# Kernel tuning notes

Measured on AMD Instinct MI355X. Metric: run time of the kernel, lower is better.

The kernel has to match this reference:

```python
import jax, jax.numpy as jnp
import numpy as np

N_NODES = 50000
N_EDGES = 800000
D = 128


def setup_inputs() -> dict:
    key = jax.random.key(0)
    ks = jax.random.split(key, 6)
    stdv = 1.0 / np.sqrt(D)
    inputs = {
        "input": jax.random.normal(ks[0], (N_NODES, D), dtype=jnp.float32),
        "h0": jax.random.normal(ks[1], (N_NODES, D), dtype=jnp.float32),
        # COO representation of the (normalized) sparse adjacency
        "vals": jax.random.uniform(ks[2], (N_EDGES,), dtype=jnp.float32) / 16.0,
        "weight": jax.random.uniform(ks[3], (D, D), dtype=jnp.float32, minval=-stdv, maxval=stdv),
        "lamda": jnp.float32(0.5),
        "alpha": jnp.float32(0.1),
        "row": jax.random.randint(ks[4], (N_EDGES,), 0, N_NODES),
        "col": jax.random.randint(ks[5], (N_EDGES,), 0, N_NODES),
        "l": 4,
    }
    return inputs


def reference(input, h0, vals, weight, lamda, alpha, row, col, l):
    # theta = log(lamda / l + 1)
    theta = jnp.log(lamda / l + 1.0)
    # hi = spmm(adj, input): gather source-node features, scale by edge
    # values, scatter-add into destination rows.  [E, D] -> [N, D]
    hi = jax.ops.segment_sum(vals[:, None] * input[col], row, num_segments=input.shape[0])
    # variant=False path
    support = (1.0 - alpha) * hi + alpha * h0
    r = support
    # output = theta * support @ W + (1 - theta) * r
    output = theta * jnp.matmul(support, weight) + (1.0 - theta) * r
    return output
```

## Files before the change

### kernel.cpp

```cpp
#include <hip/hip_runtime.h>
#include <cmath>

constexpr int N_NODES = 50000;
constexpr int N_EDGES = 800000;
constexpr int D = 128;
constexpr int CAP = 32;
constexpr int OVF_CAP = 8192;

constexpr int EPB = 2048;
constexpr int SCAT_BLOCKS = (N_EDGES + EPB - 1) / EPB;
constexpr int CAST_BLOCKS = (N_NODES * D / 8 + 255) / 256;

constexpr size_t OFF_OVFCNT = 200000;
constexpr size_t OFF_BUCKET = 200064;
constexpr size_t OFF_OVF    = 6600064;
constexpr size_t OFF_PACKED = 6731136;
constexpr size_t OFF_WT     = 19531136;

typedef __attribute__((ext_vector_type(8))) short bf16x8;
typedef __attribute__((ext_vector_type(4))) float f32x4;

__device__ __forceinline__ unsigned bf16rn(float f) {
    unsigned u = __float_as_uint(f);
    return (u + 0x7fffu + ((u >> 16) & 1u)) >> 16;
}
__device__ __forceinline__ float bf_lo(unsigned u) { return __uint_as_float(u << 16); }
__device__ __forceinline__ float bf_hi(unsigned u) { return __uint_as_float(u & 0xffff0000u); }

__device__ __forceinline__ unsigned enc_val(float v) {
    int m = (int)(v * 1048576.0f + 0.5f);
    if (m > 65535) m = 65535;
    if (m < 0) m = 0;
    return (unsigned)m;
}

__device__ __forceinline__ void push_edge(
    int r, int c, float v,
    int* __restrict__ cnt, unsigned* __restrict__ bucket,
    int* __restrict__ ovf_cnt, int4* __restrict__ ovf)
{
    unsigned ent = (unsigned)c | (enc_val(v) << 16);
    int pos = atomicAdd(&cnt[r], 1);
    if (pos < CAP) bucket[(size_t)r * CAP + pos] = ent;
    else {
        int o = atomicAdd(ovf_cnt, 1);
        if (o < OVF_CAP) ovf[o] = make_int4(r, c,
            __float_as_int((float)(ent >> 16) * (1.0f / 1048576.0f)), 0);
    }
}

__global__ __launch_bounds__(256) void scatter_cast(
    const int* __restrict__ row, const int* __restrict__ col,
    const float* __restrict__ vals, const float* __restrict__ input,
    const float* __restrict__ weight,
    int* __restrict__ cnt, unsigned* __restrict__ bucket,
    int* __restrict__ ovf_cnt, int4* __restrict__ ovf,
    unsigned* __restrict__ packed, ushort* __restrict__ wt)
{
    if (blockIdx.x < SCAT_BLOCKS) {
        const int gbase = blockIdx.x * (EPB / 4);

        #pragma unroll
        for (int it = 0; it < EPB / 4 / 256; ++it) {
            int gi = gbase + it * 256 + threadIdx.x;
            if (gi >= N_EDGES / 4) break;
            int4   r4 = ((const int4*)row)[gi];
            int4   c4 = ((const int4*)col)[gi];
            float4 v4 = ((const float4*)vals)[gi];
            push_edge(r4.x, c4.x, v4.x, cnt, bucket, ovf_cnt, ovf);
            push_edge(r4.y, c4.y, v4.y, cnt, bucket, ovf_cnt, ovf);
            push_edge(r4.z, c4.z, v4.z, cnt, bucket, ovf_cnt, ovf);
            push_edge(r4.w, c4.w, v4.w, cnt, bucket, ovf_cnt, ovf);
        }
    } else if (blockIdx.x < SCAT_BLOCKS + CAST_BLOCKS) {
        int i = (blockIdx.x - SCAT_BLOCKS) * 256 + threadIdx.x;
        if (i >= N_NODES * D / 8) return;
        const float4* f = (const float4*)(input + (size_t)i * 8);
        float4 a = f[0], b = f[1];
        uint4 o;
        o.x = bf16rn(a.x) | (bf16rn(a.y) << 16);
        o.y = bf16rn(a.z) | (bf16rn(a.w) << 16);
        o.z = bf16rn(b.x) | (bf16rn(b.y) << 16);
        o.w = bf16rn(b.z) | (bf16rn(b.w) << 16);
        ((uint4*)packed)[i] = o;
    } else {
        #pragma unroll
        for (int j = 0; j < 64; ++j) {
            int idx = threadIdx.x + j * 256;
            int k = idx >> 7, n = idx & 127;
            wt[n * 128 + k] = (ushort)bf16rn(weight[idx]);
        }
    }
}

__global__ __launch_bounds__(256) void gather_support(
    const unsigned* __restrict__ packed,
    const float* __restrict__ h0,
    const float* __restrict__ alpha_p,
    const int* __restrict__ cnt,
    const unsigned* __restrict__ bucket,
    float* __restrict__ support)
{
    const float alpha = *alpha_p;
    const float oma = 1.0f - alpha;
    const int wv   = threadIdx.x >> 6;
    const int lane = threadIdx.x & 63;
    const int q    = lane & 15;
    const int slot = lane >> 4;

    const int g = blockIdx.x * 4 + wv;
    if (g >= N_NODES) return;

    int n = cnt[g];
    if (n > CAP) n = CAP;
    const unsigned* b = bucket + (size_t)g * CAP;
    const uint4* pk = (const uint4*)packed;

    const int q4 = (n + 3) >> 2;
    const int s0 = slot * q4;
    int s1 = s0 + q4; if (s1 > n) s1 = n;

    float acc[8] = {0.f, 0.f, 0.f, 0.f, 0.f, 0.f, 0.f, 0.f};
    for (int e = s0; e < s1; e += 4) {
        int rem = s1 - e;
        unsigned m0 = b[e];
        unsigned m1 = (rem > 1) ? b[e + 1] : 0u;
        unsigned m2 = (rem > 2) ? b[e + 2] : 0u;
        unsigned m3 = (rem > 3) ? b[e + 3] : 0u;
        uint4 x0 = pk[(size_t)(m0 & 0xffffu) * 16 + q];
        uint4 x1 = pk[(size_t)(m1 & 0xffffu) * 16 + q];
        uint4 x2 = pk[(size_t)(m2 & 0xffffu) * 16 + q];
        uint4 x3 = pk[(size_t)(m3 & 0xffffu) * 16 + q];
        float v0 = (float)(m0 >> 16) * (1.0f / 1048576.0f);
        float v1 = (float)(m1 >> 16) * (1.0f / 1048576.0f);
        float v2 = (float)(m2 >> 16) * (1.0f / 1048576.0f);
        float v3 = (float)(m3 >> 16) * (1.0f / 1048576.0f);
        acc[0] += v0 * bf_lo(x0.x); acc[1] += v0 * bf_hi(x0.x);
        acc[2] += v0 * bf_lo(x0.y); acc[3] += v0 * bf_hi(x0.y);
        acc[4] += v0 * bf_lo(x0.z); acc[5] += v0 * bf_hi(x0.z);
        acc[6] += v0 * bf_lo(x0.w); acc[7] += v0 * bf_hi(x0.w);
        acc[0] += v1 * bf_lo(x1.x); acc[1] += v1 * bf_hi(x1.x);
        acc[2] += v1 * bf_lo(x1.y); acc[3] += v1 * bf_hi(x1.y);
        acc[4] += v1 * bf_lo(x1.z); acc[5] += v1 * bf_hi(x1.z);
        acc[6] += v1 * bf_lo(x1.w); acc[7] += v1 * bf_hi(x1.w);
        acc[0] += v2 * bf_lo(x2.x); acc[1] += v2 * bf_hi(x2.x);
        acc[2] += v2 * bf_lo(x2.y); acc[3] += v2 * bf_hi(x2.y);
        acc[4] += v2 * bf_lo(x2.z); acc[5] += v2 * bf_hi(x2.z);
        acc[6] += v2 * bf_lo(x2.w); acc[7] += v2 * bf_hi(x2.w);
        acc[0] += v3 * bf_lo(x3.x); acc[1] += v3 * bf_hi(x3.x);
        acc[2] += v3 * bf_lo(x3.y); acc[3] += v3 * bf_hi(x3.y);
        acc[4] += v3 * bf_lo(x3.z); acc[5] += v3 * bf_hi(x3.z);
        acc[6] += v3 * bf_lo(x3.w); acc[7] += v3 * bf_hi(x3.w);
    }
    #pragma unroll
    for (int j = 0; j < 8; ++j) {
        acc[j] += __shfl_xor(acc[j], 16);
        acc[j] += __shfl_xor(acc[j], 32);
    }
    if (slot == 0) {
        const float* hp = h0 + (size_t)g * D + q * 8;
        float4 ha = *(const float4*)(hp);
        float4 hb = *(const float4*)(hp + 4);
        float* sp = support + (size_t)g * D + q * 8;
        float4 sa, sb;
        sa.x = oma * acc[0] + alpha * ha.x;
        sa.y = oma * acc[1] + alpha * ha.y;
        sa.z = oma * acc[2] + alpha * ha.z;
        sa.w = oma * acc[3] + alpha * ha.w;
        sb.x = oma * acc[4] + alpha * hb.x;
        sb.y = oma * acc[5] + alpha * hb.y;
        sb.z = oma * acc[6] + alpha * hb.z;
        sb.w = oma * acc[7] + alpha * hb.w;
        *(float4*)(sp) = sa;
        *(float4*)(sp + 4) = sb;
    }
}

__global__ __launch_bounds__(256) void ovf_apply(
    const float* __restrict__ input,
    const float* __restrict__ alpha_p,
    const int* __restrict__ ovf_cnt,
    const int4* __restrict__ ovf,
    float* __restrict__ support)
{
    int n = *ovf_cnt;
    if (n > OVF_CAP) n = OVF_CAP;
    const float oma = 1.0f - *alpha_p;
    for (int i = blockIdx.x * 256 + threadIdx.x; i < n * 2; i += gridDim.x * 256) {
        int idx = i >> 1, part = i & 1;
        int4 m = ovf[idx];
        float v = oma * __int_as_float(m.z);
        const float* x = input + (size_t)m.y * D + part * 64;
        float* s = support + (size_t)m.x * D + part * 64;
        for (int k = 0; k < 64; ++k) atomicAdd(&s[k], v * x[k]);
    }
}

__global__ __launch_bounds__(256) void gemm_mfma(
    const ushort* __restrict__ wt,
    const float* __restrict__ lamda_p,
    const int* __restrict__ l_p,
    float* __restrict__ data)
{
    constexpr int SP = 136;
    __shared__ ushort sA[64 * SP];
    __shared__ ushort sB[128 * SP];

    const int tid = threadIdx.x;
    const float lamda = *lamda_p;
    const float theta = logf(lamda / (float)(*l_p) + 1.0f);
    const float omt = 1.0f - theta;
    const int row0 = blockIdx.x * 64;

    #pragma unroll
    for (int j = 0; j < 8; ++j) {
        int idx = j * 256 + tid;
        int n  = idx >> 4;
        int k8 = (idx & 15) << 3;
        *(uint4*)(&sB[n * SP + k8]) = ((const uint4*)wt)[idx];
    }
    #pragma unroll
    for (int j = 0; j < 8; ++j) {
        int idx = j * 256 + tid;
        int rr = idx >> 5;
        int c4 = (idx & 31) << 2;
        int g = row0 + rr;
        float4 s = make_float4(0.f, 0.f, 0.f, 0.f);
        if (g < N_NODES) s = *(const float4*)(data + (size_t)g * D + c4);
        uint2 pkv;
        pkv.x = bf16rn(s.x) | (bf16rn(s.y) << 16);
        pkv.y = bf16rn(s.z) | (bf16rn(s.w) << 16);
        *(uint2*)(&sA[rr * SP + c4]) = pkv;
    }
    __syncthreads();

    const int wave = tid >> 6;
    const int lane = tid & 63;
    const int m    = lane & 15;
    const int quad = lane >> 4;
    const int arow = wave * 16 + m;

    f32x4 acc[8] = {};
    #pragma unroll
    for (int kb = 0; kb < 4; ++kb) {
        bf16x8 a = *(const bf16x8*)(&sA[arow * SP + kb * 32 + quad * 8]);
        #pragma unroll
        for (int nt = 0; nt < 8; ++nt) {
            bf16x8 b = *(const bf16x8*)(&sB[(nt * 16 + m) * SP + kb * 32 + quad * 8]);
            acc[nt] = __builtin_amdgcn_mfma_f32_16x16x32_bf16(a, b, acc[nt], 0, 0, 0);
        }
    }

    const int gbase = row0 + wave * 16 + quad * 4;
    #pragma unroll
    for (int nt = 0; nt < 8; ++nt) {
        int colb = nt * 16 + m;
        #pragma unroll
        for (int i = 0; i < 4; ++i) {
            int g = gbase + i;
            if (g < N_NODES) {
                size_t off = (size_t)g * D + colb;
                float s = data[off];
                data[off] = theta * acc[nt][i] + omt * s;
            }
        }
    }
}

extern "C" void kernel_launch(void* const* d_in, const int* in_sizes, int n_in,
                              void* d_out, int out_size, void* d_ws, size_t ws_size,
                              hipStream_t stream) {
    const float* input  = (const float*)d_in[0];
    const float* h0     = (const float*)d_in[1];
    const float* vals   = (const float*)d_in[2];
    const float* weight = (const float*)d_in[3];
    const float* lamda  = (const float*)d_in[4];
    const float* alpha  = (const float*)d_in[5];
    const int*   row    = (const int*)d_in[6];
    const int*   col    = (const int*)d_in[7];
    const int*   l      = (const int*)d_in[8];
    float* out = (float*)d_out;

    char* ws = (char*)d_ws;
    int*      cnt     = (int*)ws;
    int*      ovf_cnt = (int*)(ws + OFF_OVFCNT);
    unsigned* bucket  = (unsigned*)(ws + OFF_BUCKET);
    int4*     ovf     = (int4*)(ws + OFF_OVF);
    unsigned* packed  = (unsigned*)(ws + OFF_PACKED);
    ushort*   wt      = (ushort*)(ws + OFF_WT);

    hipMemsetAsync(ws, 0, OFF_BUCKET, stream);

    scatter_cast<<<SCAT_BLOCKS + CAST_BLOCKS + 1, 256, 0, stream>>>(
        row, col, vals, input, weight, cnt, bucket, ovf_cnt, ovf, packed, wt);

    int gatherb = (N_NODES + 3) / 4;
    gather_support<<<gatherb, 256, 0, stream>>>(packed, h0, alpha, cnt, bucket, out);

    ovf_apply<<<8, 256, 0, stream>>>(input, alpha, ovf_cnt, ovf, out);

    int gemmb = (N_NODES + 63) / 64;
    gemm_mfma<<<gemmb, 256, 0, stream>>>(wt, lamda, l, out);
}
```

Measured before the change: 203.5 us.

## Fuse gather, overflow handling and MFMA GEMM into one kernel

Merges the sparse gather, the overflow-edge apply and the bf16 MFMA GEMM into a single kernel. Each block builds its 64 support rows directly into shared memory as bf16 and writes the (1-theta)*support residual, then adds theta*GEMM. This removes the global roundtrip of the support matrix, the atomics and two launches. The trade-off is fewer blocks with serial per-row gathering, plus a linear scan of the overflow list per row.

```diff
diff --git a/kernel.cpp b/kernel.cpp
--- a/kernel.cpp
+++ b/kernel.cpp
@@ -93,122 +93,27 @@
     }
 }
 
-__global__ __launch_bounds__(256) void gather_support(
+__global__ __launch_bounds__(256) void gather_gemm(
     const unsigned* __restrict__ packed,
     const float* __restrict__ h0,
     const float* __restrict__ alpha_p,
     const int* __restrict__ cnt,
     const unsigned* __restrict__ bucket,
-    float* __restrict__ support)
-{
-    const float alpha = *alpha_p;
-    const float oma = 1.0f - alpha;
-    const int wv   = threadIdx.x >> 6;
-    const int lane = threadIdx.x & 63;
-    const int q    = lane & 15;
-    const int slot = lane >> 4;
-
-    const int g = blockIdx.x * 4 + wv;
-    if (g >= N_NODES) return;
-
-    int n = cnt[g];
-    if (n > CAP) n = CAP;
-    const unsigned* b = bucket + (size_t)g * CAP;
-    const uint4* pk = (const uint4*)packed;
-
-    const int q4 = (n + 3) >> 2;
-    const int s0 = slot * q4;
-    int s1 = s0 + q4; if (s1 > n) s1 = n;
-
-    float acc[8] = {0.f, 0.f, 0.f, 0.f, 0.f, 0.f, 0.f, 0.f};
-    for (int e = s0; e < s1; e += 4) {
-        int rem = s1 - e;
-        unsigned m0 = b[e];
-        unsigned m1 = (rem > 1) ? b[e + 1] : 0u;
-        unsigned m2 = (rem > 2) ? b[e + 2] : 0u;
-        unsigned m3 = (rem > 3) ? b[e + 3] : 0u;
-        uint4 x0 = pk[(size_t)(m0 & 0xffffu) * 16 + q];
-        uint4 x1 = pk[(size_t)(m1 & 0xffffu) * 16 + q];
-        uint4 x2 = pk[(size_t)(m2 & 0xffffu) * 16 + q];
-        uint4 x3 = pk[(size_t)(m3 & 0xffffu) * 16 + q];
-        float v0 = (float)(m0 >> 16) * (1.0f / 1048576.0f);
-        float v1 = (float)(m1 >> 16) * (1.0f / 1048576.0f);
-        float v2 = (float)(m2 >> 16) * (1.0f / 1048576.0f);
-        float v3 = (float)(m3 >> 16) * (1.0f / 1048576.0f);
-        acc[0] += v0 * bf_lo(x0.x); acc[1] += v0 * bf_hi(x0.x);
-        acc[2] += v0 * bf_lo(x0.y); acc[3] += v0 * bf_hi(x0.y);
-        acc[4] += v0 * bf_lo(x0.z); acc[5] += v0 * bf_hi(x0.z);
-        acc[6] += v0 * bf_lo(x0.w); acc[7] += v0 * bf_hi(x0.w);
-        acc[0] += v1 * bf_lo(x1.x); acc[1] += v1 * bf_hi(x1.x);
-        acc[2] += v1 * bf_lo(x1.y); acc[3] += v1 * bf_hi(x1.y);
-        acc[4] += v1 * bf_lo(x1.z); acc[5] += v1 * bf_hi(x1.z);
-        acc[6] += v1 * bf_lo(x1.w); acc[7] += v1 * bf_hi(x1.w);
-        acc[0] += v2 * bf_lo(x2.x); acc[1] += v2 * bf_hi(x2.x);
-        acc[2] += v2 * bf_lo(x2.y); acc[3] += v2 * bf_hi(x2.y);
-        acc[4] += v2 * bf_lo(x2.z); acc[5] += v2 * bf_hi(x2.z);
-        acc[6] += v2 * bf_lo(x2.w); acc[7] += v2 * bf_hi(x2.w);
-        acc[0] += v3 * bf_lo(x3.x); acc[1] += v3 * bf_hi(x3.x);
-        acc[2] += v3 * bf_lo(x3.y); acc[3] += v3 * bf_hi(x3.y);
-        acc[4] += v3 * bf_lo(x3.z); acc[5] += v3 * bf_hi(x3.z);
-        acc[6] += v3 * bf_lo(x3.w); acc[7] += v3 * bf_hi(x3.w);
-    }
-    #pragma unroll
-    for (int j = 0; j < 8; ++j) {
-        acc[j] += __shfl_xor(acc[j], 16);
-        acc[j] += __shfl_xor(acc[j], 32);
-    }
-    if (slot == 0) {
-        const float* hp = h0 + (size_t)g * D + q * 8;
-        float4 ha = *(const float4*)(hp);
-        float4 hb = *(const float4*)(hp + 4);
-        float* sp = support + (size_t)g * D + q * 8;
-        float4 sa, sb;
-        sa.x = oma * acc[0] + alpha * ha.x;
-        sa.y = oma * acc[1] + alpha * ha.y;
-        sa.z = oma * acc[2] + alpha * ha.z;
-        sa.w = oma * acc[3] + alpha * ha.w;
-        sb.x = oma * acc[4] + alpha * hb.x;
-        sb.y = oma * acc[5] + alpha * hb.y;
-        sb.z = oma * acc[6] + alpha * hb.z;
-        sb.w = oma * acc[7] + alpha * hb.w;
-        *(float4*)(sp) = sa;
-        *(float4*)(sp + 4) = sb;
-    }
-}
-
-__global__ __launch_bounds__(256) void ovf_apply(
-    const float* __restrict__ input,
-    const float* __restrict__ alpha_p,
-    const int* __restrict__ ovf_cnt,
+    const int* __restrict__ ovf_cnt_p,
     const int4* __restrict__ ovf,
-    float* __restrict__ support)
-{
-    int n = *ovf_cnt;
-    if (n > OVF_CAP) n = OVF_CAP;
-    const float oma = 1.0f - *alpha_p;
-    for (int i = blockIdx.x * 256 + threadIdx.x; i < n * 2; i += gridDim.x * 256) {
-        int idx = i >> 1, part = i & 1;
-        int4 m = ovf[idx];
-        float v = oma * __int_as_float(m.z);
-        const float* x = input + (size_t)m.y * D + part * 64;
-        float* s = support + (size_t)m.x * D + part * 64;
-        for (int k = 0; k < 64; ++k) atomicAdd(&s[k], v * x[k]);
-    }
-}
-
-__global__ __launch_bounds__(256) void gemm_mfma(
     const ushort* __restrict__ wt,
     const float* __restrict__ lamda_p,
     const int* __restrict__ l_p,
-    float* __restrict__ data)
+    float* __restrict__ out)
 {
     constexpr int SP = 136;
     __shared__ ushort sA[64 * SP];
     __shared__ ushort sB[128 * SP];
 
     const int tid = threadIdx.x;
-    const float lamda = *lamda_p;
-    const float theta = logf(lamda / (float)(*l_p) + 1.0f);
+    const float alpha = *alpha_p;
+    const float oma = 1.0f - alpha;
+    const float theta = logf((*lamda_p) / (float)(*l_p) + 1.0f);
     const float omt = 1.0f - theta;
     const int row0 = blockIdx.x * 64;
 
@@ -219,26 +124,106 @@
         int k8 = (idx & 15) << 3;
         *(uint4*)(&sB[n * SP + k8]) = ((const uint4*)wt)[idx];
     }
-    #pragma unroll
-    for (int j = 0; j < 8; ++j) {
-        int idx = j * 256 + tid;
-        int rr = idx >> 5;
-        int c4 = (idx & 31) << 2;
-        int g = row0 + rr;
-        float4 s = make_float4(0.f, 0.f, 0.f, 0.f);
-        if (g < N_NODES) s = *(const float4*)(data + (size_t)g * D + c4);
-        uint2 pkv;
-        pkv.x = bf16rn(s.x) | (bf16rn(s.y) << 16);
-        pkv.y = bf16rn(s.z) | (bf16rn(s.w) << 16);
-        *(uint2*)(&sA[rr * SP + c4]) = pkv;
+
+    int novf = *ovf_cnt_p;
+    if (novf > OVF_CAP) novf = OVF_CAP;
+
+    const int wv   = tid >> 6;
+    const int lane = tid & 63;
+    const int q    = lane & 15;
+    const int slot = lane >> 4;
+    const uint4* pk = (const uint4*)packed;
+
+    for (int rr = 0; rr < 16; ++rr) {
+        const int g = row0 + wv * 16 + rr;
+        float acc[8] = {0.f, 0.f, 0.f, 0.f, 0.f, 0.f, 0.f, 0.f};
+
+        if (g < N_NODES) {
+            int n = cnt[g];
+            if (n > CAP) n = CAP;
+            const unsigned* b = bucket + (size_t)g * CAP;
+            const int q4 = (n + 3) >> 2;
+            const int s0 = slot * q4;
+            int s1 = s0 + q4; if (s1 > n) s1 = n;
+
+            for (int e = s0; e < s1; e += 4) {
+                int rem = s1 - e;
+                unsigned m0 = b[e];
+                unsigned m1 = (rem > 1) ? b[e + 1] : 0u;
+                unsigned m2 = (rem > 2) ? b[e + 2] : 0u;
+                unsigned m3 = (rem > 3) ? b[e + 3] : 0u;
+                uint4 x0 = pk[(size_t)(m0 & 0xffffu) * 16 + q];
+                uint4 x1 = pk[(size_t)(m1 & 0xffffu) * 16 + q];
+                uint4 x2 = pk[(size_t)(m2 & 0xffffu) * 16 + q];
+                uint4 x3 = pk[(size_t)(m3 & 0xffffu) * 16 + q];
+                float v0 = (float)(m0 >> 16) * (1.0f / 1048576.0f);
+                float v1 = (float)(m1 >> 16) * (1.0f / 1048576.0f);
+                float v2 = (float)(m2 >> 16) * (1.0f / 1048576.0f);
+                float v3 = (float)(m3 >> 16) * (1.0f / 1048576.0f);
+                acc[0] += v0 * bf_lo(x0.x); acc[1] += v0 * bf_hi(x0.x);
+                acc[2] += v0 * bf_lo(x0.y); acc[3] += v0 * bf_hi(x0.y);
+                acc[4] += v0 * bf_lo(x0.z); acc[5] += v0 * bf_hi(x0.z);
+                acc[6] += v0 * bf_lo(x0.w); acc[7] += v0 * bf_hi(x0.w);
+                acc[0] += v1 * bf_lo(x1.x); acc[1] += v1 * bf_hi(x1.x);
+                acc[2] += v1 * bf_lo(x1.y); acc[3] += v1 * bf_hi(x1.y);
+                acc[4] += v1 * bf_lo(x1.z); acc[5] += v1 * bf_hi(x1.z);
+                acc[6] += v1 * bf_lo(x1.w); acc[7] += v1 * bf_hi(x1.w);
+                acc[0] += v2 * bf_lo(x2.x); acc[1] += v2 * bf_hi(x2.x);
+                acc[2] += v2 * bf_lo(x2.y); acc[3] += v2 * bf_hi(x2.y);
+                acc[4] += v2 * bf_lo(x2.z); acc[5] += v2 * bf_hi(x2.z);
+                acc[6] += v2 * bf_lo(x2.w); acc[7] += v2 * bf_hi(x2.w);
+                acc[0] += v3 * bf_lo(x3.x); acc[1] += v3 * bf_hi(x3.x);
+                acc[2] += v3 * bf_lo(x3.y); acc[3] += v3 * bf_hi(x3.y);
+                acc[4] += v3 * bf_lo(x3.z); acc[5] += v3 * bf_hi(x3.z);
+                acc[6] += v3 * bf_lo(x3.w); acc[7] += v3 * bf_hi(x3.w);
+            }
+        }
+        #pragma unroll
+        for (int j = 0; j < 8; ++j) {
+            acc[j] += __shfl_xor(acc[j], 16);
+            acc[j] += __shfl_xor(acc[j], 32);
+        }
+        if (slot == 0) {
+            uint4 pkv = make_uint4(0, 0, 0, 0);
+            if (g < N_NODES) {
+                for (int o = 0; o < novf; ++o) {
+                    int4 m = ovf[o];
+                    if (m.x == g) {
+                        float v = __int_as_float(m.z);
+                        uint4 x = pk[(size_t)m.y * 16 + q];
+                        acc[0] += v * bf_lo(x.x); acc[1] += v * bf_hi(x.x);
+                        acc[2] += v * bf_lo(x.y); acc[3] += v * bf_hi(x.y);
+                        acc[4] += v * bf_lo(x.z); acc[5] += v * bf_hi(x.z);
+                        acc[6] += v * bf_lo(x.w); acc[7] += v * bf_hi(x.w);
+                    }
+                }
+                const float* hp = h0 + (size_t)g * D + q * 8;
+                float4 ha = *(const float4*)(hp);
+                float4 hb = *(const float4*)(hp + 4);
+                float s0 = oma * acc[0] + alpha * ha.x;
+                float s1 = oma * acc[1] + alpha * ha.y;
+                float s2 = oma * acc[2] + alpha * ha.z;
+                float s3 = oma * acc[3] + alpha * ha.w;
+                float s4 = oma * acc[4] + alpha * hb.x;
+                float s5 = oma * acc[5] + alpha * hb.y;
+                float s6 = oma * acc[6] + alpha * hb.z;
+                float s7 = oma * acc[7] + alpha * hb.w;
+                float* op = out + (size_t)g * D + q * 8;
+                *(float4*)(op)     = make_float4(omt * s0, omt * s1, omt * s2, omt * s3);
+                *(float4*)(op + 4) = make_float4(omt * s4, omt * s5, omt * s6, omt * s7);
+                pkv.x = bf16rn(s0) | (bf16rn(s1) << 16);
+                pkv.y = bf16rn(s2) | (bf16rn(s3) << 16);
+                pkv.z = bf16rn(s4) | (bf16rn(s5) << 16);
+                pkv.w = bf16rn(s6) | (bf16rn(s7) << 16);
+            }
+            *(uint4*)(&sA[(wv * 16 + rr) * SP + q * 8]) = pkv;
+        }
     }
     __syncthreads();
 
-    const int wave = tid >> 6;
-    const int lane = tid & 63;
     const int m    = lane & 15;
     const int quad = lane >> 4;
-    const int arow = wave * 16 + m;
+    const int arow = wv * 16 + m;
 
     f32x4 acc[8] = {};
     #pragma unroll
@@ -251,7 +236,7 @@
         }
     }
 
-    const int gbase = row0 + wave * 16 + quad * 4;
+    const int gbase = row0 + wv * 16 + quad * 4;
     #pragma unroll
     for (int nt = 0; nt < 8; ++nt) {
         int colb = nt * 16 + m;
@@ -260,8 +245,7 @@
             int g = gbase + i;
             if (g < N_NODES) {
                 size_t off = (size_t)g * D + colb;
-                float s = data[off];
-                data[off] = theta * acc[nt][i] + omt * s;
+                out[off] = out[off] + theta * acc[nt][i];
             }
         }
     }
@@ -294,11 +278,7 @@
     scatter_cast<<<SCAT_BLOCKS + CAST_BLOCKS + 1, 256, 0, stream>>>(
         row, col, vals, input, weight, cnt, bucket, ovf_cnt, ovf, packed, wt);
 
-    int gatherb = (N_NODES + 3) / 4;
-    gather_support<<<gatherb, 256, 0, stream>>>(packed, h0, alpha, cnt, bucket, out);
-
-    ovf_apply<<<8, 256, 0, stream>>>(input, alpha, ovf_cnt, ovf, out);
-
-    int gemmb = (N_NODES + 63) / 64;
-    gemm_mfma<<<gemmb, 256, 0, stream>>>(wt, lamda, l, out);
-}
+    int fusedb = (N_NODES + 63) / 64;
+    gather_gemm<<<fusedb, 256, 0, stream>>>(
+        packed, h0, alpha, cnt, bucket, ovf_cnt, ovf, wt, lamda, l, out);
+}
```

Result: slower. 269.0 us (+32.1%).

## Reorder to transform-then-aggregate and fuse GEMM into scatter kernel

Applied to the files above, without the earlier changes.

Uses linearity to compute Z = (1-alpha)(theta*X@W + (1-theta)X) before the sparse aggregation, plus the h0 term computed directly into out. The GEMM moves into the scatter launch as extra blocks, so the separate GEMM kernel and its read-modify-write pass over the output go away. The gather then adds aggregated bf16 Z rows into out. This runs two dense GEMMs (input and h0) instead of one, rounds Z to bf16 after the mix instead of rounding the input, and each GEMM block re-converts the weight in shared memory.

```diff
diff --git a/kernel.cpp b/kernel.cpp
--- a/kernel.cpp
+++ b/kernel.cpp
@@ -9,13 +9,12 @@
 
 constexpr int EPB = 2048;
 constexpr int SCAT_BLOCKS = (N_EDGES + EPB - 1) / EPB;
-constexpr int CAST_BLOCKS = (N_NODES * D / 8 + 255) / 256;
+constexpr int ZBLOCKS = (N_NODES + 63) / 64;
 
 constexpr size_t OFF_OVFCNT = 200000;
 constexpr size_t OFF_BUCKET = 200064;
 constexpr size_t OFF_OVF    = 6600064;
-constexpr size_t OFF_PACKED = 6731136;
-constexpr size_t OFF_WT     = 19531136;
+constexpr size_t OFF_ZP     = 6731136;
 
 typedef __attribute__((ext_vector_type(8))) short bf16x8;
 typedef __attribute__((ext_vector_type(4))) float f32x4;
@@ -44,22 +43,22 @@
     if (pos < CAP) bucket[(size_t)r * CAP + pos] = ent;
     else {
         int o = atomicAdd(ovf_cnt, 1);
-        if (o < OVF_CAP) ovf[o] = make_int4(r, c,
-            __float_as_int((float)(ent >> 16) * (1.0f / 1048576.0f)), 0);
-    }
-}
-
-__global__ __launch_bounds__(256) void scatter_cast(
+        if (o < OVF_CAP) ovf[o] = make_int4(r, c, __float_as_int(v), 0);
+    }
+}
+
+__global__ __launch_bounds__(256) void scatter_zgemm(
     const int* __restrict__ row, const int* __restrict__ col,
     const float* __restrict__ vals, const float* __restrict__ input,
-    const float* __restrict__ weight,
+    const float* __restrict__ h0, const float* __restrict__ weight,
+    const float* __restrict__ lamda_p, const float* __restrict__ alpha_p,
+    const int* __restrict__ l_p,
     int* __restrict__ cnt, unsigned* __restrict__ bucket,
     int* __restrict__ ovf_cnt, int4* __restrict__ ovf,
-    unsigned* __restrict__ packed, ushort* __restrict__ wt)
+    ushort* __restrict__ zp, float* __restrict__ out)
 {
     if (blockIdx.x < SCAT_BLOCKS) {
         const int gbase = blockIdx.x * (EPB / 4);
-
         #pragma unroll
         for (int it = 0; it < EPB / 4 / 256; ++it) {
             int gi = gbase + it * 256 + threadIdx.x;
@@ -72,37 +71,92 @@
             push_edge(r4.z, c4.z, v4.z, cnt, bucket, ovf_cnt, ovf);
             push_edge(r4.w, c4.w, v4.w, cnt, bucket, ovf_cnt, ovf);
         }
-    } else if (blockIdx.x < SCAT_BLOCKS + CAST_BLOCKS) {
-        int i = (blockIdx.x - SCAT_BLOCKS) * 256 + threadIdx.x;
-        if (i >= N_NODES * D / 8) return;
-        const float4* f = (const float4*)(input + (size_t)i * 8);
-        float4 a = f[0], b = f[1];
-        uint4 o;
-        o.x = bf16rn(a.x) | (bf16rn(a.y) << 16);
-        o.y = bf16rn(a.z) | (bf16rn(a.w) << 16);
-        o.z = bf16rn(b.x) | (bf16rn(b.y) << 16);
-        o.w = bf16rn(b.z) | (bf16rn(b.w) << 16);
-        ((uint4*)packed)[i] = o;
-    } else {
+        return;
+    }
+
+    constexpr int SP = 136;
+    __shared__ ushort sA[64 * SP];
+    __shared__ ushort sB[128 * SP];
+
+    const int bi   = blockIdx.x - SCAT_BLOCKS;
+    const bool isH = bi >= ZBLOCKS;
+    const int gb   = isH ? bi - ZBLOCKS : bi;
+    const float* src = isH ? h0 : input;
+
+    const int tid = threadIdx.x;
+    const float alpha = *alpha_p;
+    const float theta = logf((*lamda_p) / (float)(*l_p) + 1.0f);
+    const float omt = 1.0f - theta;
+    const float oscale = isH ? alpha : (1.0f - alpha);
+    const int row0 = gb * 64;
+
+    #pragma unroll
+    for (int j = 0; j < 16; ++j) {
+        int idx = j * 256 + tid;
+        float4 w = ((const float4*)weight)[idx];
+        int k  = idx >> 5;
+        int n0 = (idx & 31) << 2;
+        sB[(n0 + 0) * SP + k] = (ushort)bf16rn(w.x);
+        sB[(n0 + 1) * SP + k] = (ushort)bf16rn(w.y);
+        sB[(n0 + 2) * SP + k] = (ushort)bf16rn(w.z);
+        sB[(n0 + 3) * SP + k] = (ushort)bf16rn(w.w);
+    }
+    #pragma unroll
+    for (int j = 0; j < 8; ++j) {
+        int idx = j * 256 + tid;
+        int rr = idx >> 5;
+        int c4 = (idx & 31) << 2;
+        int g = row0 + rr;
+        float4 s = make_float4(0.f, 0.f, 0.f, 0.f);
+        if (g < N_NODES) s = *(const float4*)(src + (size_t)g * D + c4);
+        uint2 pkv;
+        pkv.x = bf16rn(s.x) | (bf16rn(s.y) << 16);
+        pkv.y = bf16rn(s.z) | (bf16rn(s.w) << 16);
+        *(uint2*)(&sA[rr * SP + c4]) = pkv;
+    }
+    __syncthreads();
+
+    const int wave = tid >> 6;
+    const int lane = tid & 63;
+    const int m    = lane & 15;
+    const int quad = lane >> 4;
+    const int arow = wave * 16 + m;
+
+    f32x4 acc[8] = {};
+    #pragma unroll
+    for (int kb = 0; kb < 4; ++kb) {
+        bf16x8 a = *(const bf16x8*)(&sA[arow * SP + kb * 32 + quad * 8]);
         #pragma unroll
-        for (int j = 0; j < 64; ++j) {
-            int idx = threadIdx.x + j * 256;
-            int k = idx >> 7, n = idx & 127;
-            wt[n * 128 + k] = (ushort)bf16rn(weight[idx]);
+        for (int nt = 0; nt < 8; ++nt) {
+            bf16x8 b = *(const bf16x8*)(&sB[(nt * 16 + m) * SP + kb * 32 + quad * 8]);
+            acc[nt] = __builtin_amdgcn_mfma_f32_16x16x32_bf16(a, b, acc[nt], 0, 0, 0);
         }
     }
-}
-
-__global__ __launch_bounds__(256) void gather_support(
-    const unsigned* __restrict__ packed,
-    const float* __restrict__ h0,
-    const float* __restrict__ alpha_p,
+
+    const int gbase = row0 + wave * 16 + quad * 4;
+    #pragma unroll
+    for (int nt = 0; nt < 8; ++nt) {
+        int c = nt * 16 + m;
+        #pragma unroll
+        for (int i = 0; i < 4; ++i) {
+            int g = gbase + i;
+            if (g < N_NODES) {
+                size_t off = (size_t)g * D + c;
+                float s = src[off];
+                float z = oscale * (theta * acc[nt][i] + omt * s);
+                if (isH) out[off] = z;
+                else     zp[off] = (ushort)bf16rn(z);
+            }
+        }
+    }
+}
+
+__global__ __launch_bounds__(256) void gather_out(
+    const ushort* __restrict__ zp,
     const int* __restrict__ cnt,
     const unsigned* __restrict__ bucket,
-    float* __restrict__ support)
-{
-    const float alpha = *alpha_p;
-    const float oma = 1.0f - alpha;
+    float* __restrict__ out)
+{
     const int wv   = threadIdx.x >> 6;
     const int lane = threadIdx.x & 63;
     const int q    = lane & 15;
@@ -114,7 +168,7 @@
     int n = cnt[g];
     if (n > CAP) n = CAP;
     const unsigned* b = bucket + (size_t)g * CAP;
-    const uint4* pk = (const uint4*)packed;
+    const uint4* pk = (const uint4*)zp;
 
     const int q4 = (n + 3) >> 2;
     const int s0 = slot * q4;
@@ -158,112 +212,32 @@
         acc[j] += __shfl_xor(acc[j], 32);
     }
     if (slot == 0) {
-        const float* hp = h0 + (size_t)g * D + q * 8;
-        float4 ha = *(const float4*)(hp);
-        float4 hb = *(const float4*)(hp + 4);
-        float* sp = support + (size_t)g * D + q * 8;
-        float4 sa, sb;
-        sa.x = oma * acc[0] + alpha * ha.x;
-        sa.y = oma * acc[1] + alpha * ha.y;
-        sa.z = oma * acc[2] + alpha * ha.z;
-        sa.w = oma * acc[3] + alpha * ha.w;
-        sb.x = oma * acc[4] + alpha * hb.x;
-        sb.y = oma * acc[5] + alpha * hb.y;
-        sb.z = oma * acc[6] + alpha * hb.z;
-        sb.w = oma * acc[7] + alpha * hb.w;
-        *(float4*)(sp) = sa;
-        *(float4*)(sp + 4) = sb;
+        float* op = out + (size_t)g * D + q * 8;
+        float4 oa = *(const float4*)(op);
+        float4 ob = *(const float4*)(op + 4);
+        oa.x += acc[0]; oa.y += acc[1]; oa.z += acc[2]; oa.w += acc[3];
+        ob.x += acc[4]; ob.y += acc[5]; ob.z += acc[6]; ob.w += acc[7];
+        *(float4*)(op)     = oa;
+        *(float4*)(op + 4) = ob;
     }
 }
 
 __global__ __launch_bounds__(256) void ovf_apply(
-    const float* __restrict__ input,
-    const float* __restrict__ alpha_p,
+    const ushort* __restrict__ zp,
     const int* __restrict__ ovf_cnt,
     const int4* __restrict__ ovf,
-    float* __restrict__ support)
+    float* __restrict__ out)
 {
     int n = *ovf_cnt;
     if (n > OVF_CAP) n = OVF_CAP;
-    const float oma = 1.0f - *alpha_p;
     for (int i = blockIdx.x * 256 + threadIdx.x; i < n * 2; i += gridDim.x * 256) {
         int idx = i >> 1, part = i & 1;
         int4 m = ovf[idx];
-        float v = oma * __int_as_float(m.z);
-        const float* x = input + (size_t)m.y * D + part * 64;
-        float* s = support + (size_t)m.x * D + part * 64;
-        for (int k = 0; k < 64; ++k) atomicAdd(&s[k], v * x[k]);
-    }
-}
-
-__global__ __launch_bounds__(256) void gemm_mfma(
-    const ushort* __restrict__ wt,
-    const float* __restrict__ lamda_p,
-    const int* __restrict__ l_p,
-    float* __restrict__ data)
-{
-    constexpr int SP = 136;
-    __shared__ ushort sA[64 * SP];
-    __shared__ ushort sB[128 * SP];
-
-    const int tid = threadIdx.x;
-    const float lamda = *lamda_p;
-    const float theta = logf(lamda / (float)(*l_p) + 1.0f);
-    const float omt = 1.0f - theta;
-    const int row0 = blockIdx.x * 64;
-
-    #pragma unroll
-    for (int j = 0; j < 8; ++j) {
-        int idx = j * 256 + tid;
-        int n  = idx >> 4;
-        int k8 = (idx & 15) << 3;
-        *(uint4*)(&sB[n * SP + k8]) = ((const uint4*)wt)[idx];
-    }
-    #pragma unroll
-    for (int j = 0; j < 8; ++j) {
-        int idx = j * 256 + tid;
-        int rr = idx >> 5;
-        int c4 = (idx & 31) << 2;
-        int g = row0 + rr;
-        float4 s = make_float4(0.f, 0.f, 0.f, 0.f);
-        if (g < N_NODES) s = *(const float4*)(data + (size_t)g * D + c4);
-        uint2 pkv;
-        pkv.x = bf16rn(s.x) | (bf16rn(s.y) << 16);
-        pkv.y = bf16rn(s.z) | (bf16rn(s.w) << 16);
-        *(uint2*)(&sA[rr * SP + c4]) = pkv;
-    }
-    __syncthreads();
-
-    const int wave = tid >> 6;
-    const int lane = tid & 63;
-    const int m    = lane & 15;
-    const int quad = lane >> 4;
-    const int arow = wave * 16 + m;
-
-    f32x4 acc[8] = {};
-    #pragma unroll
-    for (int kb = 0; kb < 4; ++kb) {
-        bf16x8 a = *(const bf16x8*)(&sA[arow * SP + kb * 32 + quad * 8]);
-        #pragma unroll
-        for (int nt = 0; nt < 8; ++nt) {
-            bf16x8 b = *(const bf16x8*)(&sB[(nt * 16 + m) * SP + kb * 32 + quad * 8]);
-            acc[nt] = __builtin_amdgcn_mfma_f32_16x16x32_bf16(a, b, acc[nt], 0, 0, 0);
-        }
-    }
-
-    const int gbase = row0 + wave * 16 + quad * 4;
-    #pragma unroll
-    for (int nt = 0; nt < 8; ++nt) {
-        int colb = nt * 16 + m;
-        #pragma unroll
-        for (int i = 0; i < 4; ++i) {
-            int g = gbase + i;
-            if (g < N_NODES) {
-                size_t off = (size_t)g * D + colb;
-                float s = data[off];
-                data[off] = theta * acc[nt][i] + omt * s;
-            }
-        }
+        float v = __int_as_float(m.z);
+        const ushort* x = zp + (size_t)m.y * D + part * 64;
+        float* s = out + (size_t)m.x * D + part * 64;
+        for (int k = 0; k < 64; ++k)
+            atomicAdd(&s[k], v * __uint_as_float((unsigned)x[k] << 16));
     }
 }
 
@@ -286,19 +260,16 @@
     int*      ovf_cnt = (int*)(ws + OFF_OVFCNT);
     unsigned* bucket  = (unsigned*)(ws + OFF_BUCKET);
     int4*     ovf     = (int4*)(ws + OFF_OVF);
-    unsigned* packed  = (unsigned*)(ws + OFF_PACKED);
-    ushort*   wt      = (ushort*)(ws + OFF_WT);
+    ushort*   zp      = (ushort*)(ws + OFF_ZP);
 
     hipMemsetAsync(ws, 0, OFF_BUCKET, stream);
 
-    scatter_cast<<<SCAT_BLOCKS + CAST_BLOCKS + 1, 256, 0, stream>>>(
-        row, col, vals, input, weight, cnt, bucket, ovf_cnt, ovf, packed, wt);
+    scatter_zgemm<<<SCAT_BLOCKS + 2 * ZBLOCKS, 256, 0, stream>>>(
+        row, col, vals, input, h0, weight, lamda, alpha, l,
+        cnt, bucket, ovf_cnt, ovf, zp, out);
 
     int gatherb = (N_NODES + 3) / 4;
-    gather_support<<<gatherb, 256, 0, stream>>>(packed, h0, alpha, cnt, bucket, out);
-
-    ovf_apply<<<8, 256, 0, stream>>>(input, alpha, ovf_cnt, ovf, out);
-
-    int gemmb = (N_NODES + 63) / 64;
-    gemm_mfma<<<gemmb, 256, 0, stream>>>(wt, lamda, l, out);
-}
+    gather_out<<<gatherb, 256, 0, stream>>>(zp, cnt, bucket, out);
+
+    ovf_apply<<<8, 256, 0, stream>>>(zp, ovf_cnt, ovf, out);
+}
```

New measurement: 217.9 us. +7.1%, slower.

## Pad per-row edge counters and fold overflow edges into the gather kernel

Applied to the files above, without the earlier changes.

Spreads each row's atomic edge counter onto its own 64-byte slot so that atomics for different rows no longer share cache lines. The workspace offsets and the zeroing memset grow to match. The separate overflow kernel, which used fp32 atomics, is removed. Instead each gather wavefront scans the short overflow list and accumulates matching edges directly, using bf16 features and the exact edge value. This saves a launch and the atomic traffic, at the cost of a larger memset and a per-row linear scan of the overflow list.

```diff
diff --git a/kernel.cpp b/kernel.cpp
--- a/kernel.cpp
+++ b/kernel.cpp
@@ -6,16 +6,17 @@
 constexpr int D = 128;
 constexpr int CAP = 32;
 constexpr int OVF_CAP = 8192;
+constexpr int CNT_STRIDE = 16;
 
 constexpr int EPB = 2048;
 constexpr int SCAT_BLOCKS = (N_EDGES + EPB - 1) / EPB;
 constexpr int CAST_BLOCKS = (N_NODES * D / 8 + 255) / 256;
 
-constexpr size_t OFF_OVFCNT = 200000;
-constexpr size_t OFF_BUCKET = 200064;
-constexpr size_t OFF_OVF    = 6600064;
-constexpr size_t OFF_PACKED = 6731136;
-constexpr size_t OFF_WT     = 19531136;
+constexpr size_t OFF_OVFCNT = 3200000;
+constexpr size_t OFF_BUCKET = 3200064;
+constexpr size_t OFF_OVF    = 9600064;
+constexpr size_t OFF_PACKED = 9731136;
+constexpr size_t OFF_WT     = 22531136;
 
 typedef __attribute__((ext_vector_type(8))) short bf16x8;
 typedef __attribute__((ext_vector_type(4))) float f32x4;
@@ -40,12 +41,11 @@
     int* __restrict__ ovf_cnt, int4* __restrict__ ovf)
 {
     unsigned ent = (unsigned)c | (enc_val(v) << 16);
-    int pos = atomicAdd(&cnt[r], 1);
+    int pos = atomicAdd(&cnt[(size_t)r * CNT_STRIDE], 1);
     if (pos < CAP) bucket[(size_t)r * CAP + pos] = ent;
     else {
         int o = atomicAdd(ovf_cnt, 1);
-        if (o < OVF_CAP) ovf[o] = make_int4(r, c,
-            __float_as_int((float)(ent >> 16) * (1.0f / 1048576.0f)), 0);
+        if (o < OVF_CAP) ovf[o] = make_int4(r, c, __float_as_int(v), 0);
     }
 }
 
@@ -59,7 +59,6 @@
 {
     if (blockIdx.x < SCAT_BLOCKS) {
         const int gbase = blockIdx.x * (EPB / 4);
-
         #pragma unroll
         for (int it = 0; it < EPB / 4 / 256; ++it) {
             int gi = gbase + it * 256 + threadIdx.x;
@@ -99,6 +98,8 @@
     const float* __restrict__ alpha_p,
     const int* __restrict__ cnt,
     const unsigned* __restrict__ bucket,
+    const int* __restrict__ ovf_cnt_p,
+    const int4* __restrict__ ovf,
     float* __restrict__ support)
 {
     const float alpha = *alpha_p;
@@ -111,7 +112,9 @@
     const int g = blockIdx.x * 4 + wv;
     if (g >= N_NODES) return;
 
-    int n = cnt[g];
+    int n = cnt[(size_t)g * CNT_STRIDE];
+    int novf = *ovf_cnt_p;
+    if (novf > OVF_CAP) novf = OVF_CAP;
     if (n > CAP) n = CAP;
     const unsigned* b = bucket + (size_t)g * CAP;
     const uint4* pk = (const uint4*)packed;
@@ -158,6 +161,17 @@
         acc[j] += __shfl_xor(acc[j], 32);
     }
     if (slot == 0) {
+        for (int o = 0; o < novf; ++o) {
+            int4 mm = ovf[o];
+            if (mm.x == g) {
+                float v = __int_as_float(mm.z);
+                uint4 x = pk[(size_t)mm.y * 16 + q];
+                acc[0] += v * bf_lo(x.x); acc[1] += v * bf_hi(x.x);
+                acc[2] += v * bf_lo(x.y); acc[3] += v * bf_hi(x.y);
+                acc[4] += v * bf_lo(x.z); acc[5] += v * bf_hi(x.z);
+                acc[6] += v * bf_lo(x.w); acc[7] += v * bf_hi(x.w);
+            }
+        }
         const float* hp = h0 + (size_t)g * D + q * 8;
         float4 ha = *(const float4*)(hp);
         float4 hb = *(const float4*)(hp + 4);
@@ -176,26 +190,6 @@
     }
 }
 
-__global__ __launch_bounds__(256) void ovf_apply(
-    const float* __restrict__ input,
-    const float* __restrict__ alpha_p,
-    const int* __restrict__ ovf_cnt,
-    const int4* __restrict__ ovf,
-    float* __restrict__ support)
-{
-    int n = *ovf_cnt;
-    if (n > OVF_CAP) n = OVF_CAP;
-    const float oma = 1.0f - *alpha_p;
-    for (int i = blockIdx.x * 256 + threadIdx.x; i < n * 2; i += gridDim.x * 256) {
-        int idx = i >> 1, part = i & 1;
-        int4 m = ovf[idx];
-        float v = oma * __int_as_float(m.z);
-        const float* x = input + (size_t)m.y * D + part * 64;
-        float* s = support + (size_t)m.x * D + part * 64;
-        for (int k = 0; k < 64; ++k) atomicAdd(&s[k], v * x[k]);
-    }
-}
-
 __global__ __launch_bounds__(256) void gemm_mfma(
     const ushort* __restrict__ wt,
     const float* __restrict__ lamda_p,
@@ -295,9 +289,8 @@
         row, col, vals, input, weight, cnt, bucket, ovf_cnt, ovf, packed, wt);
 
     int gatherb = (N_NODES + 3) / 4;
-    gather_support<<<gatherb, 256, 0, stream>>>(packed, h0, alpha, cnt, bucket, out);
-
-    ovf_apply<<<8, 256, 0, stream>>>(input, alpha, ovf_cnt, ovf, out);
+    gather_support<<<gatherb, 256, 0, stream>>>(
+        packed, h0, alpha, cnt, bucket, ovf_cnt, ovf, out);
 
     int gemmb = (N_NODES + 63) / 64;
     gemm_mfma<<<gemmb, 256, 0, stream>>>(wt, lamda, l, out);
```

Result: no change. 204.6 us (+0.5%).
